# Kernel optimization log

Measured on AMD Instinct MI355X. Metric: run time of the kernel, lower is better.

Reference implementation:

```python
import jax, jax.numpy as jnp
import numpy as np

E = 1_000_000
D = 64
N = 100_000


def setup_inputs() -> dict:
    key = jax.random.key(0)
    k1, k2 = jax.random.split(key)
    mj = jax.random.normal(k1, (E, D), dtype=jnp.float32)
    edge_index = jax.random.randint(k2, (2, E), 0, N, dtype=jnp.int64)
    return {"mj": mj, "edge_index": edge_index, "num_nodes": N}


def reference(mj, edge_index, num_nodes):
    # source_to_target=True: scatter-add edge features into target nodes (edge_index[1])
    # mj: [E, D], edge_index: [2, E] -> vi: [num_nodes, D]
    vi = jax.ops.segment_sum(mj, edge_index[1, :], num_segments=num_nodes)
    return vi
```

## Files before the change

kernel.cpp:

```cpp
#include <hip/hip_runtime.h>


typedef float f4 __attribute__((ext_vector_type(4)));

#define FEAT 64
#define CAP 32
#define OVF_CAP (1 << 20)

__global__ void __launch_bounds__(256)
scatter_kernel(const int* __restrict__ tgt, int* __restrict__ cursor,
               int* __restrict__ bucket, int* __restrict__ ovf_cnt,
               int* __restrict__ ovf, int E) {
    int i = blockIdx.x * 256 + threadIdx.x;
    if (i >= E) return;
    int t = tgt[i];
    int pos = atomicAdd(&cursor[t], 1);
    if (pos < CAP) {
        bucket[t * CAP + pos] = i;
    } else {
        int q = atomicAdd(ovf_cnt, 1);
        if (q < OVF_CAP) { ovf[2 * q] = t; ovf[2 * q + 1] = i; }
    }
}

__global__ void __launch_bounds__(256)
gather_kernel(const f4* __restrict__ mj4, const int* __restrict__ cursor,
              const int* __restrict__ bucket, f4* __restrict__ out4, int N) {
    int gid = (blockIdx.x * 256 + threadIdx.x) >> 4;
    int l = threadIdx.x & 15;
    if (gid >= N) return;
    int deg = cursor[gid];
    if (deg > CAP) deg = CAP;
    const int* row = bucket + gid * CAP;
    f4 acc = {0.f, 0.f, 0.f, 0.f};
    int j = 0;
    for (; j + 3 < deg; j += 4) {
        int e0 = row[j], e1 = row[j + 1], e2 = row[j + 2], e3 = row[j + 3];
        f4 a = mj4[(size_t)e0 * 16 + l];
        f4 b = mj4[(size_t)e1 * 16 + l];
        f4 c = mj4[(size_t)e2 * 16 + l];
        f4 d = mj4[(size_t)e3 * 16 + l];
        acc += a + b + c + d;
    }
    for (; j < deg; ++j) {
        acc += mj4[(size_t)row[j] * 16 + l];
    }
    out4[(size_t)gid * 16 + l] = acc;
}

__global__ void __launch_bounds__(256)
cleanup_kernel(const float* __restrict__ mj, const int* __restrict__ ovf_cnt,
               const int* __restrict__ ovf, float* __restrict__ out) {
    int n = *ovf_cnt;
    if (n > OVF_CAP) n = OVF_CAP;
    int sub = threadIdx.x >> 6;
    int lane = threadIdx.x & 63;
    for (int k = sub; k < n; k += 4) {
        int t = ovf[2 * k], e = ovf[2 * k + 1];
        atomicAdd(&out[(size_t)t * FEAT + lane], mj[(size_t)e * FEAT + lane]);
    }
}

extern "C" void kernel_launch(void* const* d_in, const int* in_sizes, int n_in,
                              void* d_out, int out_size, void* d_ws, size_t ws_size,
                              hipStream_t stream) {
    const float* mj = (const float*)d_in[0];
    const int* edge_index = (const int*)d_in[1];
    int E = in_sizes[1] / 2;
    const int* tgt = edge_index + E;
    int N = out_size / FEAT;

    int* cursor  = (int*)d_ws;
    int* ovf_cnt = cursor + N;
    int* ovf     = ovf_cnt + 1;
    int* bucket  = ovf + 2 * OVF_CAP;

    hipMemsetAsync(cursor, 0, (size_t)(N + 1) * sizeof(int), stream);

    int eblk = (E + 255) / 256;
    scatter_kernel<<<eblk, 256, 0, stream>>>(tgt, cursor, bucket, ovf_cnt, ovf, E);

    int gblk = (N * 16 + 255) / 256;
    gather_kernel<<<gblk, 256, 0, stream>>>(
        (const f4*)mj, cursor, bucket, (f4*)d_out, N);

    cleanup_kernel<<<1, 256, 0, stream>>>(mj, ovf_cnt, ovf, (float*)d_out);
}
```

Before: 127.2 us.

## Fold overflow handling into gather and vectorize scatter and index loads

Drops the separate single-block cleanup kernel and instead has each gather group scan the overflow list for its own node, saving a launch and a serialized tail. The scatter kernel now reads targets as int4 and handles four edges per thread. The gather kernel loads bucket indices as int4 and unrolls by eight to keep more gathers in flight. The trade-offs: an overflow scan that is linear in the overflow count for every node, which is costly if overflow is ever large, and fewer scatter threads each issuing four serial atomics.

```diff
diff --git a/kernel.cpp b/kernel.cpp
--- a/kernel.cpp
+++ b/kernel.cpp
@@ -8,57 +8,73 @@
 #define OVF_CAP (1 << 20)
 
 __global__ void __launch_bounds__(256)
-scatter_kernel(const int* __restrict__ tgt, int* __restrict__ cursor,
+scatter_kernel(const int4* __restrict__ tgt4, int* __restrict__ cursor,
                int* __restrict__ bucket, int* __restrict__ ovf_cnt,
                int* __restrict__ ovf, int E) {
     int i = blockIdx.x * 256 + threadIdx.x;
-    if (i >= E) return;
-    int t = tgt[i];
-    int pos = atomicAdd(&cursor[t], 1);
-    if (pos < CAP) {
-        bucket[t * CAP + pos] = i;
-    } else {
-        int q = atomicAdd(ovf_cnt, 1);
-        if (q < OVF_CAP) { ovf[2 * q] = t; ovf[2 * q + 1] = i; }
+    int base = i * 4;
+    if (base >= E) return;
+    int4 t4 = tgt4[i];
+    int t[4] = {t4.x, t4.y, t4.z, t4.w};
+#pragma unroll
+    for (int k = 0; k < 4; ++k) {
+        if (base + k < E) {
+            int pos = atomicAdd(&cursor[t[k]], 1);
+            if (pos < CAP) {
+                bucket[t[k] * CAP + pos] = base + k;
+            } else {
+                int q = atomicAdd(ovf_cnt, 1);
+                if (q < OVF_CAP) { ovf[2 * q] = t[k]; ovf[2 * q + 1] = base + k; }
+            }
+        }
     }
 }
 
 __global__ void __launch_bounds__(256)
 gather_kernel(const f4* __restrict__ mj4, const int* __restrict__ cursor,
-              const int* __restrict__ bucket, f4* __restrict__ out4, int N) {
+              const int* __restrict__ bucket, const int* __restrict__ ovf_cnt,
+              const int* __restrict__ ovf, f4* __restrict__ out4, int N) {
     int gid = (blockIdx.x * 256 + threadIdx.x) >> 4;
     int l = threadIdx.x & 15;
     if (gid >= N) return;
     int deg = cursor[gid];
     if (deg > CAP) deg = CAP;
     const int* row = bucket + gid * CAP;
+    const int4* row4 = (const int4*)row;
     f4 acc = {0.f, 0.f, 0.f, 0.f};
     int j = 0;
+    for (; j + 7 < deg; j += 8) {
+        int4 ea = row4[j >> 2];
+        int4 eb = row4[(j >> 2) + 1];
+        f4 v0 = mj4[(size_t)ea.x * 16 + l];
+        f4 v1 = mj4[(size_t)ea.y * 16 + l];
+        f4 v2 = mj4[(size_t)ea.z * 16 + l];
+        f4 v3 = mj4[(size_t)ea.w * 16 + l];
+        f4 v4 = mj4[(size_t)eb.x * 16 + l];
+        f4 v5 = mj4[(size_t)eb.y * 16 + l];
+        f4 v6 = mj4[(size_t)eb.z * 16 + l];
+        f4 v7 = mj4[(size_t)eb.w * 16 + l];
+        acc += ((v0 + v1) + (v2 + v3)) + ((v4 + v5) + (v6 + v7));
+    }
     for (; j + 3 < deg; j += 4) {
-        int e0 = row[j], e1 = row[j + 1], e2 = row[j + 2], e3 = row[j + 3];
-        f4 a = mj4[(size_t)e0 * 16 + l];
-        f4 b = mj4[(size_t)e1 * 16 + l];
-        f4 c = mj4[(size_t)e2 * 16 + l];
-        f4 d = mj4[(size_t)e3 * 16 + l];
-        acc += a + b + c + d;
+        int4 ea = row4[j >> 2];
+        f4 v0 = mj4[(size_t)ea.x * 16 + l];
+        f4 v1 = mj4[(size_t)ea.y * 16 + l];
+        f4 v2 = mj4[(size_t)ea.z * 16 + l];
+        f4 v3 = mj4[(size_t)ea.w * 16 + l];
+        acc += (v0 + v1) + (v2 + v3);
     }
     for (; j < deg; ++j) {
         acc += mj4[(size_t)row[j] * 16 + l];
     }
+    int n = *ovf_cnt;
+    if (n > 0) {
+        if (n > OVF_CAP) n = OVF_CAP;
+        for (int k = 0; k < n; ++k) {
+            if (ovf[2 * k] == gid) acc += mj4[(size_t)ovf[2 * k + 1] * 16 + l];
+        }
+    }
     out4[(size_t)gid * 16 + l] = acc;
-}
-
-__global__ void __launch_bounds__(256)
-cleanup_kernel(const float* __restrict__ mj, const int* __restrict__ ovf_cnt,
-               const int* __restrict__ ovf, float* __restrict__ out) {
-    int n = *ovf_cnt;
-    if (n > OVF_CAP) n = OVF_CAP;
-    int sub = threadIdx.x >> 6;
-    int lane = threadIdx.x & 63;
-    for (int k = sub; k < n; k += 4) {
-        int t = ovf[2 * k], e = ovf[2 * k + 1];
-        atomicAdd(&out[(size_t)t * FEAT + lane], mj[(size_t)e * FEAT + lane]);
-    }
 }
 
 extern "C" void kernel_launch(void* const* d_in, const int* in_sizes, int n_in,
@@ -72,17 +88,17 @@
 
     int* cursor  = (int*)d_ws;
     int* ovf_cnt = cursor + N;
-    int* ovf     = ovf_cnt + 1;
+    int* ovf     = cursor + N + 4;
     int* bucket  = ovf + 2 * OVF_CAP;
 
-    hipMemsetAsync(cursor, 0, (size_t)(N + 1) * sizeof(int), stream);
+    hipMemsetAsync(cursor, 0, (size_t)(N + 4) * sizeof(int), stream);
 
-    int eblk = (E + 255) / 256;
-    scatter_kernel<<<eblk, 256, 0, stream>>>(tgt, cursor, bucket, ovf_cnt, ovf, E);
+    int e4 = (E + 3) / 4;
+    int eblk = (e4 + 255) / 256;
+    scatter_kernel<<<eblk, 256, 0, stream>>>(
+        (const int4*)tgt, cursor, bucket, ovf_cnt, ovf, E);
 
     int gblk = (N * 16 + 255) / 256;
     gather_kernel<<<gblk, 256, 0, stream>>>(
-        (const f4*)mj, cursor, bucket, (f4*)d_out, N);
-
-    cleanup_kernel<<<1, 256, 0, stream>>>(mj, ovf_cnt, ovf, (float*)d_out);
+        (const f4*)mj, cursor, bucket, ovf_cnt, ovf, (f4*)d_out, N);
 }
```

Measured after the change: 131.8 us. +3.6%, slower.

## Fuse memset, bucket scatter, gather and overflow into one cooperative kernel

Applied to the files above, without the earlier changes.

Replaces the memset plus three kernel launches with a single cooperative persistent kernel that zeroes counters, scatters edge ids into per-node buckets, and gathers sums, separated by grid-wide syncs. Overflow edges are now handled inside the gather by scanning the overflow list per node instead of a separate atomic cleanup kernel, and bucket rows are read as int4. This removes launch and memset overhead at the cost of grid syncs and a fixed grid of 1024 blocks. The per-node linear overflow scan could become very expensive if many nodes exceed the bucket capacity.

```diff
diff --git a/kernel.cpp b/kernel.cpp
--- a/kernel.cpp
+++ b/kernel.cpp
@@ -1,63 +1,70 @@
 #include <hip/hip_runtime.h>
+#include <hip/hip_cooperative_groups.h>
 
+
+namespace cg = cooperative_groups;
 
 typedef float f4 __attribute__((ext_vector_type(4)));
 
 #define FEAT 64
 #define CAP 32
 #define OVF_CAP (1 << 20)
+#define NT 256
+#define NB 1024
 
-__global__ void __launch_bounds__(256)
-scatter_kernel(const int* __restrict__ tgt, int* __restrict__ cursor,
-               int* __restrict__ bucket, int* __restrict__ ovf_cnt,
-               int* __restrict__ ovf, int E) {
-    int i = blockIdx.x * 256 + threadIdx.x;
-    if (i >= E) return;
-    int t = tgt[i];
-    int pos = atomicAdd(&cursor[t], 1);
-    if (pos < CAP) {
-        bucket[t * CAP + pos] = i;
-    } else {
-        int q = atomicAdd(ovf_cnt, 1);
-        if (q < OVF_CAP) { ovf[2 * q] = t; ovf[2 * q + 1] = i; }
+__global__ void __launch_bounds__(NT)
+fused_kernel(const f4* __restrict__ mj4, const int* __restrict__ tgt,
+             int* __restrict__ cursor, int* __restrict__ bucket,
+             int* __restrict__ ovf_cnt, int* __restrict__ ovf,
+             f4* __restrict__ out4, int E, int N) {
+    cg::grid_group grid = cg::this_grid();
+    int tid = blockIdx.x * NT + threadIdx.x;
+    int nthr = gridDim.x * NT;
+
+    for (int i = tid; i < N + 4; i += nthr) cursor[i] = 0;
+    grid.sync();
+
+    for (int i = tid; i < E; i += nthr) {
+        int t = tgt[i];
+        int pos = atomicAdd(&cursor[t], 1);
+        if (pos < CAP) {
+            bucket[t * CAP + pos] = i;
+        } else {
+            int q = atomicAdd(ovf_cnt, 1);
+            if (q < OVF_CAP) { ovf[2 * q] = t; ovf[2 * q + 1] = i; }
+        }
     }
-}
+    __threadfence();
+    grid.sync();
 
-__global__ void __launch_bounds__(256)
-gather_kernel(const f4* __restrict__ mj4, const int* __restrict__ cursor,
-              const int* __restrict__ bucket, f4* __restrict__ out4, int N) {
-    int gid = (blockIdx.x * 256 + threadIdx.x) >> 4;
-    int l = threadIdx.x & 15;
-    if (gid >= N) return;
-    int deg = cursor[gid];
-    if (deg > CAP) deg = CAP;
-    const int* row = bucket + gid * CAP;
-    f4 acc = {0.f, 0.f, 0.f, 0.f};
-    int j = 0;
-    for (; j + 3 < deg; j += 4) {
-        int e0 = row[j], e1 = row[j + 1], e2 = row[j + 2], e3 = row[j + 3];
-        f4 a = mj4[(size_t)e0 * 16 + l];
-        f4 b = mj4[(size_t)e1 * 16 + l];
-        f4 c = mj4[(size_t)e2 * 16 + l];
-        f4 d = mj4[(size_t)e3 * 16 + l];
-        acc += a + b + c + d;
-    }
-    for (; j < deg; ++j) {
-        acc += mj4[(size_t)row[j] * 16 + l];
-    }
-    out4[(size_t)gid * 16 + l] = acc;
-}
-
-__global__ void __launch_bounds__(256)
-cleanup_kernel(const float* __restrict__ mj, const int* __restrict__ ovf_cnt,
-               const int* __restrict__ ovf, float* __restrict__ out) {
-    int n = *ovf_cnt;
-    if (n > OVF_CAP) n = OVF_CAP;
-    int sub = threadIdx.x >> 6;
-    int lane = threadIdx.x & 63;
-    for (int k = sub; k < n; k += 4) {
-        int t = ovf[2 * k], e = ovf[2 * k + 1];
-        atomicAdd(&out[(size_t)t * FEAT + lane], mj[(size_t)e * FEAT + lane]);
+    int l = tid & 15;
+    int ngrp = nthr >> 4;
+    int novf = *ovf_cnt;
+    if (novf > OVF_CAP) novf = OVF_CAP;
+    for (int gid = tid >> 4; gid < N; gid += ngrp) {
+        int deg = cursor[gid];
+        if (deg > CAP) deg = CAP;
+        const int* row = bucket + gid * CAP;
+        const int4* row4 = (const int4*)row;
+        f4 acc = {0.f, 0.f, 0.f, 0.f};
+        int j = 0;
+        for (; j + 3 < deg; j += 4) {
+            int4 ea = row4[j >> 2];
+            f4 v0 = mj4[(size_t)ea.x * 16 + l];
+            f4 v1 = mj4[(size_t)ea.y * 16 + l];
+            f4 v2 = mj4[(size_t)ea.z * 16 + l];
+            f4 v3 = mj4[(size_t)ea.w * 16 + l];
+            acc += (v0 + v1) + (v2 + v3);
+        }
+        for (; j < deg; ++j) {
+            acc += mj4[(size_t)row[j] * 16 + l];
+        }
+        if (novf > 0) {
+            for (int k = 0; k < novf; ++k) {
+                if (ovf[2 * k] == gid) acc += mj4[(size_t)ovf[2 * k + 1] * 16 + l];
+            }
+        }
+        out4[(size_t)gid * 16 + l] = acc;
     }
 }
 
@@ -67,22 +74,20 @@
     const float* mj = (const float*)d_in[0];
     const int* edge_index = (const int*)d_in[1];
     int E = in_sizes[1] / 2;
-    const int* tgt = edge_index + E;
+    const int* tgt_p = edge_index + E;
     int N = out_size / FEAT;
 
     int* cursor  = (int*)d_ws;
     int* ovf_cnt = cursor + N;
-    int* ovf     = ovf_cnt + 1;
+    int* ovf     = cursor + N + 4;
     int* bucket  = ovf + 2 * OVF_CAP;
 
-    hipMemsetAsync(cursor, 0, (size_t)(N + 1) * sizeof(int), stream);
+    const f4* mj4 = (const f4*)mj;
+    f4* out4 = (f4*)d_out;
 
-    int eblk = (E + 255) / 256;
-    scatter_kernel<<<eblk, 256, 0, stream>>>(tgt, cursor, bucket, ovf_cnt, ovf, E);
-
-    int gblk = (N * 16 + 255) / 256;
-    gather_kernel<<<gblk, 256, 0, stream>>>(
-        (const f4*)mj, cursor, bucket, (f4*)d_out, N);
-
-    cleanup_kernel<<<1, 256, 0, stream>>>(mj, ovf_cnt, ovf, (float*)d_out);
+    void* args[] = {(void*)&mj4, (void*)&tgt_p, (void*)&cursor, (void*)&bucket,
+                    (void*)&ovf_cnt, (void*)&ovf, (void*)&out4,
+                    (void*)&E, (void*)&N};
+    hipLaunchCooperativeKernel((const void*)fused_kernel, dim3(NB), dim3(NT),
+                               args, 0, stream);
 }
```

Measured after the change: 408.4 us. 3.21x slower.
